# Kernel tuning notes

Hardware: AMD Instinct MI355X
Metric: run time of the kernel (lower is better)

Reference implementation:

```python
import jax, jax.numpy as jnp
import numpy as np

B, C, H, W = 32, 256, 64, 64
HID = 16  # max(8, 256 // 16)


def setup_inputs() -> dict:
    key = jax.random.key(0)
    k1, k2, k3 = jax.random.split(key, 3)
    x = jax.random.normal(k1, (B, C, H, W), dtype=jnp.float32)
    # 1x1 conv weights (kernel spatial dims squeezed away)
    w1 = jax.random.normal(k2, (HID, C), dtype=jnp.float32) * (1.0 / np.sqrt(C))
    b1 = jnp.zeros((HID,), dtype=jnp.float32)
    w2 = jax.random.normal(k3, (C, HID), dtype=jnp.float32) * (1.0 / np.sqrt(HID))
    b2 = jnp.zeros((C,), dtype=jnp.float32)
    return {"x": x, "w1": w1, "b1": b1, "w2": w2, "b2": b2}


def reference(x, w1, b1, w2, b2):
    # Squeeze: global average pool over H, W -> [B, C]
    s = jnp.mean(x, axis=(2, 3))
    # Excite: two 1x1 convs on a [B,C,1,1] tensor == channel-wise MLP
    h = jax.nn.relu(jnp.einsum('bc,hc->bh', s, w1) + b1)          # [B, HID]
    g = jax.nn.sigmoid(jnp.einsum('bh,ch->bc', h, w2) + b2)       # [B, C]
    # Scale: broadcast gate over spatial dims
    return x * g[:, :, None, None]
```

## Files before the change

kernel.cpp:

```cpp
#include <hip/hip_runtime.h>
#include <math.h>

#define SE_B   32
#define SE_C   256
#define SE_HID 16
#define SE_HW  4096
#define SE_HW4 1024

typedef float f4v __attribute__((ext_vector_type(4)));

__global__ __launch_bounds__(256) void se_mean_kernel(const float* __restrict__ x,
                                                      float* __restrict__ s) {
    const int wave = threadIdx.x >> 6;
    const int lane = threadIdx.x & 63;
    const int plane = blockIdx.x * 4 + wave;

    const float4* xp = (const float4*)x + (size_t)plane * SE_HW4;

    float sum = 0.f;
#pragma unroll
    for (int k = 0; k < 16; ++k) {
        float4 v = xp[lane + k * 64];
        sum += (v.x + v.y) + (v.z + v.w);
    }
#pragma unroll
    for (int off = 32; off > 0; off >>= 1) sum += __shfl_down(sum, off, 64);

    if (lane == 0) s[plane] = sum * (1.0f / SE_HW);
}

__global__ __launch_bounds__(256) void se_gate_kernel(const float* __restrict__ s,
                                                      const float* __restrict__ w1,
                                                      const float* __restrict__ b1,
                                                      const float* __restrict__ w2,
                                                      const float* __restrict__ b2,
                                                      float* __restrict__ g) {
    const int b = blockIdx.x;
    const int tid = threadIdx.x;

    __shared__ float s_sh[SE_C];
    __shared__ float part[16][17];
    __shared__ float h_sh[SE_HID];

    s_sh[tid] = s[b * SE_C + tid];
    __syncthreads();

    const int i = tid & 15;
    const int j = tid >> 4;
    {
        const float* wrow = w1 + i * SE_C + j * 16;
        const float* srow = s_sh + j * 16;
        float p = 0.f;
#pragma unroll
        for (int k = 0; k < 16; ++k) p = fmaf(srow[k], wrow[k], p);
        part[j][i] = p;
    }
    __syncthreads();

    if (tid < SE_HID) {
        float acc = b1[tid];
#pragma unroll
        for (int k = 0; k < 16; ++k) acc += part[k][tid];
        h_sh[tid] = fmaxf(acc, 0.f);
    }
    __syncthreads();

    {
        float acc = b2[tid];
        const float* w2r = w2 + tid * SE_HID;
#pragma unroll
        for (int k = 0; k < 16; ++k) acc = fmaf(h_sh[k], w2r[k], acc);
        g[b * SE_C + tid] = 1.0f / (1.0f + expf(-acc));
    }
}

__global__ __launch_bounds__(256) void se_apply_kernel(const float* __restrict__ x,
                                                       const float* __restrict__ g,
                                                       float* __restrict__ out) {
    const int wave = threadIdx.x >> 6;
    const int lane = threadIdx.x & 63;
    const int plane = blockIdx.x * 4 + wave;

    const float gv = g[plane];
    const float4* xp = (const float4*)x + (size_t)plane * SE_HW4;
    float4* op = (float4*)out + (size_t)plane * SE_HW4;

    float4 v[16];
#pragma unroll
    for (int k = 0; k < 16; ++k) v[k] = xp[lane + k * 64];

#pragma unroll
    for (int k = 0; k < 16; ++k) {
        v[k].x *= gv; v[k].y *= gv; v[k].z *= gv; v[k].w *= gv;
        __builtin_nontemporal_store(*(f4v*)&v[k], (f4v*)(op + lane + k * 64));
    }
}

extern "C" void kernel_launch(void* const* d_in, const int* in_sizes, int n_in,
                              void* d_out, int out_size, void* d_ws, size_t ws_size,
                              hipStream_t stream) {
    const float* x  = (const float*)d_in[0];
    const float* w1 = (const float*)d_in[1];
    const float* b1 = (const float*)d_in[2];
    const float* w2 = (const float*)d_in[3];
    const float* b2 = (const float*)d_in[4];
    float* out = (float*)d_out;

    float* s = (float*)d_ws;
    float* g = (float*)d_ws + SE_B * SE_C;

    se_mean_kernel<<<SE_B * SE_C / 4, 256, 0, stream>>>(x, s);
    se_gate_kernel<<<SE_B, 256, 0, stream>>>(s, w1, b1, w2, b2, g);
    se_apply_kernel<<<SE_B * SE_C / 4, 256, 0, stream>>>(x, g, out);
}
```

Measured before the change: 257.5 us.

## Fuse gate MLP into apply kernel, computing gate per wave redundantly

Removes the separate tiny gate kernel and its launch. Each wave of the apply kernel now recomputes the hidden layer and its channel's sigmoid gate directly from the pooled means using shuffles. The apply loop is split into two halves of 8 float4 loads to reduce register pressure, and the mean kernel now accumulates into four independent partial sums. The cost is redundant MLP work in every wave (extra loads of w1 and s) in exchange for one fewer launch and one fewer serialization point.

```diff
diff --git a/kernel.cpp b/kernel.cpp
--- a/kernel.cpp
+++ b/kernel.cpp
@@ -17,82 +17,73 @@
 
     const float4* xp = (const float4*)x + (size_t)plane * SE_HW4;
 
-    float sum = 0.f;
+    float4 acc = {0.f, 0.f, 0.f, 0.f};
 #pragma unroll
     for (int k = 0; k < 16; ++k) {
         float4 v = xp[lane + k * 64];
-        sum += (v.x + v.y) + (v.z + v.w);
+        acc.x += v.x; acc.y += v.y; acc.z += v.z; acc.w += v.w;
     }
+    float sum = (acc.x + acc.y) + (acc.z + acc.w);
 #pragma unroll
     for (int off = 32; off > 0; off >>= 1) sum += __shfl_down(sum, off, 64);
 
     if (lane == 0) s[plane] = sum * (1.0f / SE_HW);
 }
 
-__global__ __launch_bounds__(256) void se_gate_kernel(const float* __restrict__ s,
-                                                      const float* __restrict__ w1,
-                                                      const float* __restrict__ b1,
-                                                      const float* __restrict__ w2,
-                                                      const float* __restrict__ b2,
-                                                      float* __restrict__ g) {
-    const int b = blockIdx.x;
-    const int tid = threadIdx.x;
-
-    __shared__ float s_sh[SE_C];
-    __shared__ float part[16][17];
-    __shared__ float h_sh[SE_HID];
-
-    s_sh[tid] = s[b * SE_C + tid];
-    __syncthreads();
-
-    const int i = tid & 15;
-    const int j = tid >> 4;
-    {
-        const float* wrow = w1 + i * SE_C + j * 16;
-        const float* srow = s_sh + j * 16;
-        float p = 0.f;
-#pragma unroll
-        for (int k = 0; k < 16; ++k) p = fmaf(srow[k], wrow[k], p);
-        part[j][i] = p;
-    }
-    __syncthreads();
-
-    if (tid < SE_HID) {
-        float acc = b1[tid];
-#pragma unroll
-        for (int k = 0; k < 16; ++k) acc += part[k][tid];
-        h_sh[tid] = fmaxf(acc, 0.f);
-    }
-    __syncthreads();
-
-    {
-        float acc = b2[tid];
-        const float* w2r = w2 + tid * SE_HID;
-#pragma unroll
-        for (int k = 0; k < 16; ++k) acc = fmaf(h_sh[k], w2r[k], acc);
-        g[b * SE_C + tid] = 1.0f / (1.0f + expf(-acc));
-    }
-}
-
-__global__ __launch_bounds__(256) void se_apply_kernel(const float* __restrict__ x,
-                                                       const float* __restrict__ g,
-                                                       float* __restrict__ out) {
+__global__ __launch_bounds__(256) void se_gate_apply_kernel(const float* __restrict__ x,
+                                                            const float* __restrict__ s,
+                                                            const float* __restrict__ w1,
+                                                            const float* __restrict__ b1,
+                                                            const float* __restrict__ w2,
+                                                            const float* __restrict__ b2,
+                                                            float* __restrict__ out) {
     const int wave = threadIdx.x >> 6;
     const int lane = threadIdx.x & 63;
     const int plane = blockIdx.x * 4 + wave;
+    const int b = plane >> 8;
+    const int c = plane & 255;
 
-    const float gv = g[plane];
+    const int i = lane & 15;
+    const int j = lane >> 4;
+
+    const float4* srow = (const float4*)(s + b * SE_C) + j * 16;
+    const float4* wrow = (const float4*)(w1 + i * SE_C) + j * 16;
+    float p = 0.f;
+#pragma unroll
+    for (int k = 0; k < 16; ++k) {
+        float4 sv = srow[k];
+        float4 wv = wrow[k];
+        p = fmaf(sv.x, wv.x, p);
+        p = fmaf(sv.y, wv.y, p);
+        p = fmaf(sv.z, wv.z, p);
+        p = fmaf(sv.w, wv.w, p);
+    }
+    p += __shfl_xor(p, 16, 64);
+    p += __shfl_xor(p, 32, 64);
+    const float h = fmaxf(p + b1[i], 0.f);
+
+    float t = h * w2[c * SE_HID + i];
+#pragma unroll
+    for (int off = 8; off > 0; off >>= 1) t += __shfl_xor(t, off, 64);
+    const float gv = 1.0f / (1.0f + expf(-(t + b2[c])));
+
     const float4* xp = (const float4*)x + (size_t)plane * SE_HW4;
     float4* op = (float4*)out + (size_t)plane * SE_HW4;
 
-    float4 v[16];
+    float4 v[8];
 #pragma unroll
-    for (int k = 0; k < 16; ++k) v[k] = xp[lane + k * 64];
-
+    for (int k = 0; k < 8; ++k) v[k] = xp[lane + k * 64];
 #pragma unroll
-    for (int k = 0; k < 16; ++k) {
+    for (int k = 0; k < 8; ++k) {
         v[k].x *= gv; v[k].y *= gv; v[k].z *= gv; v[k].w *= gv;
         __builtin_nontemporal_store(*(f4v*)&v[k], (f4v*)(op + lane + k * 64));
+    }
+#pragma unroll
+    for (int k = 0; k < 8; ++k) v[k] = xp[lane + (k + 8) * 64];
+#pragma unroll
+    for (int k = 0; k < 8; ++k) {
+        v[k].x *= gv; v[k].y *= gv; v[k].z *= gv; v[k].w *= gv;
+        __builtin_nontemporal_store(*(f4v*)&v[k], (f4v*)(op + lane + (k + 8) * 64));
     }
 }
 
@@ -107,9 +98,7 @@
     float* out = (float*)d_out;
 
     float* s = (float*)d_ws;
-    float* g = (float*)d_ws + SE_B * SE_C;
 
     se_mean_kernel<<<SE_B * SE_C / 4, 256, 0, stream>>>(x, s);
-    se_gate_kernel<<<SE_B, 256, 0, stream>>>(s, w1, b1, w2, b2, g);
-    se_apply_kernel<<<SE_B * SE_C / 4, 256, 0, stream>>>(x, g, out);
+    se_gate_apply_kernel<<<SE_B * SE_C / 4, 256, 0, stream>>>(x, s, w1, b1, w2, b2, out);
 }
```

Result: no change. 257.4 us (-0.0%).
